# Optimization experiments

Hardware: AMD Instinct MI355X
Metric: run time of the kernel (lower is better)

## Reference

```python
import jax, jax.numpy as jnp
import numpy as np

MAX_BOXES = 50
NOOBJ_SCALE = 1.0
OBJ_SCALE = 5.0
COORD_SCALE = 1.0
CLASS_SCALE = 1.0
SIL_THRESH = 0.6


def setup_inputs() -> dict:
    key = jax.random.key(0)
    k1, k2, k3, k4 = jax.random.split(key, 4)
    nB, nA, nC, nH, nW = 32, 5, 20, 64, 64
    output = jax.random.normal(k1, (nB, nA * (5 + nC), nH, nW), jnp.float32) * 0.5
    # targets: 12 valid boxes per image, rest zero (loop-break semantics)
    K = 12
    cls = jax.random.randint(k2, (nB, MAX_BOXES, 1), 0, nC).astype(jnp.float32)
    xy = jax.random.uniform(k3, (nB, MAX_BOXES, 2), minval=0.05, maxval=0.95)
    wh = jax.random.uniform(k4, (nB, MAX_BOXES, 2), minval=0.05, maxval=0.3)
    boxes = jnp.concatenate([cls, xy, wh], axis=-1)          # [nB, 50, 5]
    valid = (jnp.arange(MAX_BOXES) < K)[None, :, None].astype(jnp.float32)
    target = (boxes * valid).reshape(nB, MAX_BOXES * 5)
    anchors = jnp.array([1.3221, 1.73145, 3.19275, 4.00944, 5.05587,
                         8.09892, 9.47112, 4.84053, 11.2364, 10.0071], jnp.float32)
    return {"output": output, "target": target, "anchors": anchors}


def _iou(b1, b2):
    # center-format boxes (cx, cy, w, h) on the last axis, broadcastable
    l = jnp.maximum(b1[..., 0] - b1[..., 2] * 0.5, b2[..., 0] - b2[..., 2] * 0.5)
    r = jnp.minimum(b1[..., 0] + b1[..., 2] * 0.5, b2[..., 0] + b2[..., 2] * 0.5)
    t = jnp.maximum(b1[..., 1] - b1[..., 3] * 0.5, b2[..., 1] - b2[..., 3] * 0.5)
    b = jnp.minimum(b1[..., 1] + b1[..., 3] * 0.5, b2[..., 1] + b2[..., 3] * 0.5)
    inter = jnp.clip(r - l, 0.0) * jnp.clip(b - t, 0.0)
    union = b1[..., 2] * b1[..., 3] + b2[..., 2] * b2[..., 3] - inter
    return inter / jnp.maximum(union, 1e-10)


def reference(output, target, anchors):
    nB, _, nH, nW = output.shape
    nA = anchors.shape[0] // 2
    nC = output.shape[1] // nA - 5
    out = output.reshape(nB, nA, 5 + nC, nH, nW)

    x = jax.nn.sigmoid(out[:, :, 0])            # [nB,nA,nH,nW]
    y = jax.nn.sigmoid(out[:, :, 1])
    w = out[:, :, 2]
    h = out[:, :, 3]
    conf = jax.nn.sigmoid(out[:, :, 4])
    cls_logits = jnp.transpose(out[:, :, 5:], (0, 1, 3, 4, 2))  # [nB,nA,nH,nW,nC]

    aw = anchors[0::2]
    ah = anchors[1::2]
    grid_x = jnp.arange(nW, dtype=output.dtype)
    grid_y = jnp.arange(nH, dtype=output.dtype)[:, None]
    px = x + grid_x
    py = y + grid_y
    pw = jnp.exp(w) * aw[None, :, None, None]
    ph = jnp.exp(h) * ah[None, :, None, None]
    # build_targets consumes pred_boxes.data -> no grad through it
    pred = jax.lax.stop_gradient(jnp.stack([px, py, pw, ph], axis=-1))  # [nB,nA,nH,nW,4]

    tgt = target.reshape(nB, -1, 5)             # (cls, x, y, w, h)
    T = tgt.shape[1]
    valid = tgt[:, :, 1] > 0
    gx = tgt[:, :, 1] * nW
    gy = tgt[:, :, 2] * nH
    gw = tgt[:, :, 3] * nW
    gh = tgt[:, :, 4] * nH
    gboxes = jnp.stack([gx, gy, gw, gh], axis=-1)  # [nB,T,4]

    # conf_mask: zero out anchors whose IoU with any gt exceeds sil_thresh
    pred_flat = pred.reshape(nB, nA * nH * nW, 4)
    ious = _iou(pred_flat[:, :, None, :], gboxes[:, None, :, :])   # [nB,nAnchors,T]
    max_iou = jnp.max(jnp.where(valid[:, None, :], ious, 0.0), axis=-1)
    conf_base = jnp.where(max_iou.reshape(nB, nA, nH, nW) > SIL_THRESH, 0.0, NOOBJ_SCALE)

    # best anchor per gt: IoU of (0,0,gw,gh) vs (0,0,aw,ah)
    inter_a = jnp.minimum(gw[..., None], aw) * jnp.minimum(gh[..., None], ah)
    iou_a = inter_a / jnp.maximum(gw[..., None] * gh[..., None] + aw * ah - inter_a, 1e-10)
    best_n = jnp.argmax(iou_a, axis=-1)          # [nB,T]

    gi = jnp.clip(jnp.floor(gx), 0, nW - 1).astype(jnp.int32)
    gj = jnp.clip(jnp.floor(gy), 0, nH - 1).astype(jnp.int32)
    bidx = jnp.arange(nB)[:, None]
    N = nB * nA * nH * nW
    flat = ((bidx * nA + best_n) * nH + gj) * nW + gi
    flat = jnp.where(valid, flat, N).reshape(-1)   # invalid gts go to dummy slot N

    def scat(base, vals):
        padded = jnp.concatenate([base.reshape(-1), jnp.zeros((1,), base.dtype)])
        return padded.at[flat].set(vals.reshape(-1))[:N].reshape(nB, nA, nH, nW)

    zeros4 = jnp.zeros((nB, nA, nH, nW), output.dtype)
    half4 = jnp.full((nB, nA, nH, nW), 0.5, output.dtype)
    # seen < 12800 branch: coord_mask all ones, tx=ty=0.5, tw=th=0 as base
    coord_mask = jnp.ones((nB, nA, nH, nW), output.dtype)
    tx = scat(half4, gx - gi.astype(output.dtype))
    ty = scat(half4, gy - gj.astype(output.dtype))
    tw = scat(zeros4, jnp.log(jnp.maximum(gw, 1e-10) / aw[best_n]))
    th = scat(zeros4, jnp.log(jnp.maximum(gh, 1e-10) / ah[best_n]))
    cls_mask = scat(zeros4, jnp.ones((nB, T), output.dtype))
    conf_mask = scat(conf_base, jnp.full((nB, T), OBJ_SCALE, output.dtype))

    pred_pad = jnp.concatenate([pred.reshape(N, 4), jnp.zeros((1, 4), pred.dtype)])
    psel = pred_pad[flat]                         # [nB*T,4]
    iou_gt = _iou(gboxes.reshape(-1, 4), psel)
    tconf = scat(zeros4, iou_gt)
    tcls = scat(zeros4, tgt[:, :, 0])

    tx, ty, tw, th, tconf = map(jax.lax.stop_gradient, (tx, ty, tw, th, tconf))

    cm = coord_mask
    loss_x = COORD_SCALE * 0.5 * jnp.sum((x * cm - tx * cm) ** 2)
    loss_y = COORD_SCALE * 0.5 * jnp.sum((y * cm - ty * cm) ** 2)
    loss_w = COORD_SCALE * 0.5 * jnp.sum((w * cm - tw * cm) ** 2)
    loss_h = COORD_SCALE * 0.5 * jnp.sum((h * cm - th * cm) ** 2)
    sq = jnp.sqrt(conf_mask)
    loss_conf = 0.5 * jnp.sum((conf * sq - tconf * sq) ** 2)
    logp = jax.nn.log_softmax(cls_logits, axis=-1)
    picked = jnp.take_along_axis(logp, tcls.astype(jnp.int32)[..., None], axis=-1)[..., 0]
    loss_cls = CLASS_SCALE * (-(picked * cls_mask).sum())
    return loss_x + loss_y + loss_w + loss_h + loss_conf + loss_cls
```

## Files before the change

### kernel.cpp

```cpp
#include <hip/hip_runtime.h>
#include <math.h>

#define NB 32
#define NA 5
#define NC 20
#define NH 64
#define NW 64
#define MAXB 50
#define CPB (NA * NH * NW)
#define NTOT (NB * CPB)
#define NBLK_DENSE (NTOT / 256)
#define NPART (NBLK_DENSE + NB)
#define SIL_THRESH 0.6f
#define OBJ_SCALE 5.0f

__device__ __forceinline__ float sigmoidf(float v) { return 1.0f / (1.0f + expf(-v)); }

__device__ __forceinline__ float iou_xywh(float x1, float y1, float w1, float h1,
                                          float x2, float y2, float w2, float h2) {
    float l = fmaxf(x1 - 0.5f * w1, x2 - 0.5f * w2);
    float r = fminf(x1 + 0.5f * w1, x2 + 0.5f * w2);
    float t = fmaxf(y1 - 0.5f * h1, y2 - 0.5f * h2);
    float b = fminf(y1 + 0.5f * h1, y2 + 0.5f * h2);
    float inter = fmaxf(r - l, 0.0f) * fmaxf(b - t, 0.0f);
    float uni = w1 * h1 + w2 * h2 - inter;
    return inter / fmaxf(uni, 1e-10f);
}

__global__ __launch_bounds__(256) void region_dense(
        const float* __restrict__ out, const float* __restrict__ target,
        const float* __restrict__ anchors, float* __restrict__ ws) {
    __shared__ float s_gx[MAXB], s_gy[MAXB], s_gw[MAXB], s_gh[MAXB];
    __shared__ int s_nv;
    __shared__ float s_aw[NA], s_ah[NA];
    __shared__ float s_part[4];

    const int tid = threadIdx.x;
    const int n = blockIdx.x * 256 + tid;
    const int b = n / CPB;

    if (tid == 0) {
        const float* tg = target + b * MAXB * 5;
        int nv = 0;
        for (int t = 0; t < MAXB; ++t) {
            float tx = tg[t * 5 + 1];
            if (tx > 0.0f) {
                s_gx[nv] = tx * NW;
                s_gy[nv] = tg[t * 5 + 2] * NH;
                s_gw[nv] = tg[t * 5 + 3] * NW;
                s_gh[nv] = tg[t * 5 + 4] * NH;
                ++nv;
            }
        }
        s_nv = nv;
    }
    if (tid < NA) { s_aw[tid] = anchors[2 * tid]; s_ah[tid] = anchors[2 * tid + 1]; }
    __syncthreads();

    const int r  = n - b * CPB;
    const int a  = r >> 12;
    const int ji = r & 4095;
    const int j  = ji >> 6;
    const int i  = ji & 63;

    const float* base = out + ((size_t)(b * 125 + a * 25) << 12) + ji;
    float xr = base[0];
    float yr = base[1 * 4096];
    float wr = base[2 * 4096];
    float hr = base[3 * 4096];
    float cr = base[4 * 4096];

    float x = sigmoidf(xr);
    float y = sigmoidf(yr);
    float conf = sigmoidf(cr);
    float px = x + (float)i;
    float py = y + (float)j;
    float pw = expf(wr) * s_aw[a];
    float ph = expf(hr) * s_ah[a];

    float maxi = 0.0f;
    const int nv = s_nv;
    for (int k = 0; k < nv; ++k) {
        float iou = iou_xywh(px, py, pw, ph, s_gx[k], s_gy[k], s_gw[k], s_gh[k]);
        maxi = fmaxf(maxi, iou);
    }
    float conf_base = (maxi > SIL_THRESH) ? 0.0f : 1.0f;

    float dx = x - 0.5f, dy = y - 0.5f;
    float v = 0.5f * (dx * dx + dy * dy + wr * wr + hr * hr)
            + 0.5f * conf_base * conf * conf;

    for (int off = 32; off; off >>= 1) v += __shfl_down(v, off);
    if ((tid & 63) == 0) s_part[tid >> 6] = v;
    __syncthreads();
    if (tid == 0)
        ws[blockIdx.x] = s_part[0] + s_part[1] + s_part[2] + s_part[3];
}

__global__ __launch_bounds__(64) void region_boxes(
        const float* __restrict__ out, const float* __restrict__ target,
        const float* __restrict__ anchors, float* __restrict__ ws) {
    const int b = blockIdx.x;
    const int tid = threadIdx.x;

    __shared__ float s_t[MAXB * 5];
    __shared__ int s_flat[MAXB];
    __shared__ float s_gx[MAXB], s_gy[MAXB], s_gw[MAXB], s_gh[MAXB];
    __shared__ int s_valid[MAXB];

    const float* tg = target + b * MAXB * 5;
    for (int idx = tid; idx < MAXB * 5; idx += 64) s_t[idx] = tg[idx];
    __syncthreads();

    float aw_[NA], ah_[NA];
    for (int q = 0; q < NA; ++q) { aw_[q] = anchors[2 * q]; ah_[q] = anchors[2 * q + 1]; }

    int myflat = -1, best_n = 0, gi = 0, gj = 0;
    float gx = 0, gy = 0, gw = 0, gh = 0, clsf = 0;
    if (tid < MAXB) {
        clsf = s_t[tid * 5 + 0];
        float xx = s_t[tid * 5 + 1];
        gx = xx * NW;
        gy = s_t[tid * 5 + 2] * NH;
        gw = s_t[tid * 5 + 3] * NW;
        gh = s_t[tid * 5 + 4] * NH;
        s_gx[tid] = gx; s_gy[tid] = gy; s_gw[tid] = gw; s_gh[tid] = gh;
        int valid = (xx > 0.0f) ? 1 : 0;
        s_valid[tid] = valid;
        if (valid) {
            float besti = -1.0f;
            for (int q = 0; q < NA; ++q) {
                float inter = fminf(gw, aw_[q]) * fminf(gh, ah_[q]);
                float iou = inter / fmaxf(gw * gh + aw_[q] * ah_[q] - inter, 1e-10f);
                if (iou > besti) { besti = iou; best_n = q; }
            }
            gi = min(max((int)floorf(gx), 0), NW - 1);
            gj = min(max((int)floorf(gy), 0), NH - 1);
            myflat = (best_n << 12) + (gj << 6) + gi;
        }
        s_flat[tid] = myflat;
    } else {
        s_flat[tid < MAXB ? tid : 0] = s_flat[tid < MAXB ? tid : 0];
    }
    __syncthreads();

    bool winner = (myflat >= 0);
    if (winner) {
        for (int t2 = tid + 1; t2 < MAXB; ++t2)
            if (s_flat[t2] == myflat) { winner = false; break; }
    }

    float delta = 0.0f;
    if (winner) {
        const float* basep = out + ((size_t)(b * 125 + best_n * 25) << 12) + (gj << 6) + gi;
        float xr = basep[0];
        float yr = basep[1 * 4096];
        float wr = basep[2 * 4096];
        float hr = basep[3 * 4096];
        float cr = basep[4 * 4096];

        float x = sigmoidf(xr);
        float y = sigmoidf(yr);
        float conf = sigmoidf(cr);
        float px = x + (float)gi;
        float py = y + (float)gj;
        float pw = expf(wr) * aw_[best_n];
        float ph = expf(hr) * ah_[best_n];

        float maxi = 0.0f;
        for (int k = 0; k < MAXB; ++k) {
            if (s_valid[k]) {
                float iou = iou_xywh(px, py, pw, ph, s_gx[k], s_gy[k], s_gw[k], s_gh[k]);
                maxi = fmaxf(maxi, iou);
            }
        }
        float conf_base = (maxi > SIL_THRESH) ? 0.0f : 1.0f;

        float txv = gx - (float)gi;
        float tyv = gy - (float)gj;
        float twv = logf(fmaxf(gw, 1e-10f) / aw_[best_n]);
        float thv = logf(fmaxf(gh, 1e-10f) / ah_[best_n]);
        float tconf = iou_xywh(gx, gy, gw, gh, px, py, pw, ph);

        float dxn = x - txv, dyn = y - tyv, dwn = wr - twv, dhn = hr - thv;
        float dxo = x - 0.5f, dyo = y - 0.5f;
        float dc = conf - tconf;

        delta = 0.5f * ((dxn * dxn - dxo * dxo) + (dyn * dyn - dyo * dyo)
                      + (dwn * dwn - wr * wr) + (dhn * dhn - hr * hr))
              + 0.5f * (OBJ_SCALE * dc * dc - conf_base * conf * conf);

        const float* cl = basep + 5 * 4096;
        int ci = (int)clsf;
        float m = -INFINITY;
        for (int c = 0; c < NC; ++c) m = fmaxf(m, cl[c * 4096]);
        float s = 0.0f;
        for (int c = 0; c < NC; ++c) s += expf(cl[c * 4096] - m);
        float picked = cl[ci * 4096] - m - logf(s);
        delta -= picked;
    }

    for (int off = 32; off; off >>= 1) delta += __shfl_down(delta, off);
    if (tid == 0) ws[NBLK_DENSE + b] = delta;
}

__global__ __launch_bounds__(256) void region_reduce(
        const float* __restrict__ ws, float* __restrict__ loss) {
    __shared__ float s_part[4];
    const int tid = threadIdx.x;
    float v = 0.0f;
    for (int idx = tid; idx < NPART; idx += 256) v += ws[idx];
    for (int off = 32; off; off >>= 1) v += __shfl_down(v, off);
    if ((tid & 63) == 0) s_part[tid >> 6] = v;
    __syncthreads();
    if (tid == 0) loss[0] = s_part[0] + s_part[1] + s_part[2] + s_part[3];
}

extern "C" void kernel_launch(void* const* d_in, const int* in_sizes, int n_in,
                              void* d_out, int out_size, void* d_ws, size_t ws_size,
                              hipStream_t stream) {
    (void)in_sizes; (void)n_in; (void)ws_size; (void)out_size;
    const float* output  = (const float*)d_in[0];
    const float* target  = (const float*)d_in[1];
    const float* anchors = (const float*)d_in[2];
    float* ws = (float*)d_ws;
    float* loss = (float*)d_out;

    region_dense<<<NBLK_DENSE, 256, 0, stream>>>(output, target, anchors, ws);
    region_boxes<<<NB, 64, 0, stream>>>(output, target, anchors, ws);
    region_reduce<<<1, 256, 0, stream>>>(ws, loss);
}
```

Before: 124.8 us.

## Precompute box edges, division-free IoU threshold test, fuse final reduction

Ground-truth boxes are now compacted once per image in a prep kernel that stores their edges and scaled areas, so dense blocks no longer rebuild them serially in thread 0. The IoU > 0.6 check becomes a division-free comparison, inter > 0.375*(area_p + area_g). Each dense thread handles two cells, and a last-block atomic counter does the final reduction, which removes the third launch. Fast intrinsics (__expf, rcp, __logf) stand in for the precise math calls, trading small accuracy differences for cheaper arithmetic.

```diff
diff --git a/kernel.cpp b/kernel.cpp
--- a/kernel.cpp
+++ b/kernel.cpp
@@ -7,16 +7,23 @@
 #define NH 64
 #define NW 64
 #define MAXB 50
-#define CPB (NA * NH * NW)
-#define NTOT (NB * CPB)
-#define NBLK_DENSE (NTOT / 256)
-#define NPART (NBLK_DENSE + NB)
-#define SIL_THRESH 0.6f
+#define CPB 20480
+#define CELLS_PER_BLOCK 512
+#define BLOCKS_PER_BATCH 40
+#define NBLK_DENSE 1280
 #define OBJ_SCALE 5.0f
-
-__device__ __forceinline__ float sigmoidf(float v) { return 1.0f / (1.0f + expf(-v)); }
-
-__device__ __forceinline__ float iou_xywh(float x1, float y1, float w1, float h1,
+#define SILC 0.375f
+
+#define WS_PART 8192
+#define NPART 1312
+#define WS_INT 9504
+#define WS_CTR (WS_INT + 32)
+
+__device__ __forceinline__ float fsig(float v) {
+    return __builtin_amdgcn_rcpf(1.0f + __expf(-v));
+}
+
+__device__ __forceinline__ float iou_full(float x1, float y1, float w1, float h1,
                                           float x2, float y2, float w2, float h2) {
     float l = fmaxf(x1 - 0.5f * w1, x2 - 0.5f * w2);
     float r = fminf(x1 + 0.5f * w1, x2 + 0.5f * w2);
@@ -27,106 +34,36 @@
     return inter / fmaxf(uni, 1e-10f);
 }
 
-__global__ __launch_bounds__(256) void region_dense(
-        const float* __restrict__ out, const float* __restrict__ target,
-        const float* __restrict__ anchors, float* __restrict__ ws) {
-    __shared__ float s_gx[MAXB], s_gy[MAXB], s_gw[MAXB], s_gh[MAXB];
-    __shared__ int s_nv;
-    __shared__ float s_aw[NA], s_ah[NA];
-    __shared__ float s_part[4];
-
-    const int tid = threadIdx.x;
-    const int n = blockIdx.x * 256 + tid;
-    const int b = n / CPB;
-
-    if (tid == 0) {
-        const float* tg = target + b * MAXB * 5;
-        int nv = 0;
-        for (int t = 0; t < MAXB; ++t) {
-            float tx = tg[t * 5 + 1];
-            if (tx > 0.0f) {
-                s_gx[nv] = tx * NW;
-                s_gy[nv] = tg[t * 5 + 2] * NH;
-                s_gw[nv] = tg[t * 5 + 3] * NW;
-                s_gh[nv] = tg[t * 5 + 4] * NH;
-                ++nv;
-            }
-        }
-        s_nv = nv;
-    }
-    if (tid < NA) { s_aw[tid] = anchors[2 * tid]; s_ah[tid] = anchors[2 * tid + 1]; }
-    __syncthreads();
-
-    const int r  = n - b * CPB;
-    const int a  = r >> 12;
-    const int ji = r & 4095;
-    const int j  = ji >> 6;
-    const int i  = ji & 63;
-
-    const float* base = out + ((size_t)(b * 125 + a * 25) << 12) + ji;
-    float xr = base[0];
-    float yr = base[1 * 4096];
-    float wr = base[2 * 4096];
-    float hr = base[3 * 4096];
-    float cr = base[4 * 4096];
-
-    float x = sigmoidf(xr);
-    float y = sigmoidf(yr);
-    float conf = sigmoidf(cr);
-    float px = x + (float)i;
-    float py = y + (float)j;
-    float pw = expf(wr) * s_aw[a];
-    float ph = expf(hr) * s_ah[a];
-
-    float maxi = 0.0f;
-    const int nv = s_nv;
-    for (int k = 0; k < nv; ++k) {
-        float iou = iou_xywh(px, py, pw, ph, s_gx[k], s_gy[k], s_gw[k], s_gh[k]);
-        maxi = fmaxf(maxi, iou);
-    }
-    float conf_base = (maxi > SIL_THRESH) ? 0.0f : 1.0f;
-
-    float dx = x - 0.5f, dy = y - 0.5f;
-    float v = 0.5f * (dx * dx + dy * dy + wr * wr + hr * hr)
-            + 0.5f * conf_base * conf * conf;
-
-    for (int off = 32; off; off >>= 1) v += __shfl_down(v, off);
-    if ((tid & 63) == 0) s_part[tid >> 6] = v;
-    __syncthreads();
-    if (tid == 0)
-        ws[blockIdx.x] = s_part[0] + s_part[1] + s_part[2] + s_part[3];
-}
-
-__global__ __launch_bounds__(64) void region_boxes(
+__global__ __launch_bounds__(64) void region_prep(
         const float* __restrict__ out, const float* __restrict__ target,
         const float* __restrict__ anchors, float* __restrict__ ws) {
     const int b = blockIdx.x;
     const int tid = threadIdx.x;
 
     __shared__ float s_t[MAXB * 5];
-    __shared__ int s_flat[MAXB];
-    __shared__ float s_gx[MAXB], s_gy[MAXB], s_gw[MAXB], s_gh[MAXB];
-    __shared__ int s_valid[MAXB];
+    __shared__ float s_e[250];
+    __shared__ int s_flat[64];
 
     const float* tg = target + b * MAXB * 5;
     for (int idx = tid; idx < MAXB * 5; idx += 64) s_t[idx] = tg[idx];
-    __syncthreads();
+    for (int idx = tid; idx < 250; idx += 64) s_e[idx] = 0.0f;
 
     float aw_[NA], ah_[NA];
     for (int q = 0; q < NA; ++q) { aw_[q] = anchors[2 * q]; ah_[q] = anchors[2 * q + 1]; }
-
-    int myflat = -1, best_n = 0, gi = 0, gj = 0;
+    __syncthreads();
+
+    bool valid = false;
+    int best_n = 0, gi = 0, gj = 0, myflat = -1;
     float gx = 0, gy = 0, gw = 0, gh = 0, clsf = 0;
+    float bl = 0, br_ = 0, bt = 0, bb_ = 0, ga = 0;
     if (tid < MAXB) {
         clsf = s_t[tid * 5 + 0];
         float xx = s_t[tid * 5 + 1];
-        gx = xx * NW;
-        gy = s_t[tid * 5 + 2] * NH;
-        gw = s_t[tid * 5 + 3] * NW;
-        gh = s_t[tid * 5 + 4] * NH;
-        s_gx[tid] = gx; s_gy[tid] = gy; s_gw[tid] = gw; s_gh[tid] = gh;
-        int valid = (xx > 0.0f) ? 1 : 0;
-        s_valid[tid] = valid;
+        gx = xx * (float)NW;
+        gy = s_t[tid * 5 + 2] * (float)NH;
+        gw = s_t[tid * 5 + 3] * (float)NW;
+        gh = s_t[tid * 5 + 4] * (float)NH;
+        valid = xx > 0.0f;
         if (valid) {
             float besti = -1.0f;
             for (int q = 0; q < NA; ++q) {
@@ -136,13 +73,29 @@
             }
             gi = min(max((int)floorf(gx), 0), NW - 1);
             gj = min(max((int)floorf(gy), 0), NH - 1);
-            myflat = (best_n << 12) + (gj << 6) + gi;
+            myflat = (best_n << 12) | (gj << 6) | gi;
+            bl = gx - 0.5f * gw; br_ = gx + 0.5f * gw;
+            bt = gy - 0.5f * gh; bb_ = gy + 0.5f * gh;
+            ga = gw * gh;
         }
-        s_flat[tid] = myflat;
-    } else {
-        s_flat[tid < MAXB ? tid : 0] = s_flat[tid < MAXB ? tid : 0];
-    }
-    __syncthreads();
+    }
+    s_flat[tid] = myflat;
+
+    unsigned long long mask = __ballot(valid);
+    int pos = __popcll(mask & ((1ull << tid) - 1ull));
+    int nv = __popcll(mask);
+    if (valid) {
+        s_e[pos] = bl; s_e[50 + pos] = br_; s_e[100 + pos] = bt;
+        s_e[150 + pos] = bb_; s_e[200 + pos] = SILC * ga;
+    }
+    __syncthreads();
+
+    float* wb = ws + b * 256;
+    for (int idx = tid; idx < 250; idx += 64) wb[idx] = s_e[idx];
+    if (tid == 0) {
+        ((int*)ws)[WS_INT + b] = nv;
+        if (b == 0) ((int*)ws)[WS_CTR] = 0;
+    }
 
     bool winner = (myflat >= 0);
     if (winner) {
@@ -159,28 +112,30 @@
         float hr = basep[3 * 4096];
         float cr = basep[4 * 4096];
 
-        float x = sigmoidf(xr);
-        float y = sigmoidf(yr);
-        float conf = sigmoidf(cr);
-        float px = x + (float)gi;
-        float py = y + (float)gj;
-        float pw = expf(wr) * aw_[best_n];
-        float ph = expf(hr) * ah_[best_n];
-
-        float maxi = 0.0f;
-        for (int k = 0; k < MAXB; ++k) {
-            if (s_valid[k]) {
-                float iou = iou_xywh(px, py, pw, ph, s_gx[k], s_gy[k], s_gw[k], s_gh[k]);
-                maxi = fmaxf(maxi, iou);
-            }
+        float x = fsig(xr), y = fsig(yr), conf = fsig(cr);
+        float aw = aw_[best_n], ah = ah_[best_n];
+        float pw = __expf(wr) * aw, ph = __expf(hr) * ah;
+        float px = x + (float)gi, py = y + (float)gj;
+        float pl = px - 0.5f * pw, pr2 = px + 0.5f * pw;
+        float pt = py - 0.5f * ph, pb2 = py + 0.5f * ph;
+        float pa375 = SILC * (pw * ph);
+
+        bool hit = false;
+        for (int k = 0; k < nv; ++k) {
+            float l = fmaxf(pl, s_e[k]);
+            float r = fminf(pr2, s_e[50 + k]);
+            float t = fmaxf(pt, s_e[100 + k]);
+            float bo = fminf(pb2, s_e[150 + k]);
+            float inter = fmaxf(r - l, 0.0f) * fmaxf(bo - t, 0.0f);
+            hit = hit || (inter > pa375 + s_e[200 + k]);
         }
-        float conf_base = (maxi > SIL_THRESH) ? 0.0f : 1.0f;
+        float cb = hit ? 0.0f : 1.0f;
 
         float txv = gx - (float)gi;
         float tyv = gy - (float)gj;
-        float twv = logf(fmaxf(gw, 1e-10f) / aw_[best_n]);
-        float thv = logf(fmaxf(gh, 1e-10f) / ah_[best_n]);
-        float tconf = iou_xywh(gx, gy, gw, gh, px, py, pw, ph);
+        float twv = __logf(fmaxf(gw, 1e-10f) / aw);
+        float thv = __logf(fmaxf(gh, 1e-10f) / ah);
+        float tconf = iou_full(gx, gy, gw, gh, px, py, pw, ph);
 
         float dxn = x - txv, dyn = y - tyv, dwn = wr - twv, dhn = hr - thv;
         float dxo = x - 0.5f, dyo = y - 0.5f;
@@ -188,32 +143,101 @@
 
         delta = 0.5f * ((dxn * dxn - dxo * dxo) + (dyn * dyn - dyo * dyo)
                       + (dwn * dwn - wr * wr) + (dhn * dhn - hr * hr))
-              + 0.5f * (OBJ_SCALE * dc * dc - conf_base * conf * conf);
+              + 0.5f * (OBJ_SCALE * dc * dc - cb * conf * conf);
 
         const float* cl = basep + 5 * 4096;
+        float lg[NC];
+        float m = -INFINITY;
+        for (int c = 0; c < NC; ++c) { lg[c] = cl[c * 4096]; m = fmaxf(m, lg[c]); }
+        float s = 0.0f;
+        for (int c = 0; c < NC; ++c) s += __expf(lg[c] - m);
         int ci = (int)clsf;
-        float m = -INFINITY;
-        for (int c = 0; c < NC; ++c) m = fmaxf(m, cl[c * 4096]);
-        float s = 0.0f;
-        for (int c = 0; c < NC; ++c) s += expf(cl[c * 4096] - m);
-        float picked = cl[ci * 4096] - m - logf(s);
-        delta -= picked;
+        delta -= (lg[ci] - m - __logf(s));
     }
 
     for (int off = 32; off; off >>= 1) delta += __shfl_down(delta, off);
-    if (tid == 0) ws[NBLK_DENSE + b] = delta;
-}
-
-__global__ __launch_bounds__(256) void region_reduce(
-        const float* __restrict__ ws, float* __restrict__ loss) {
-    __shared__ float s_part[4];
+    if (tid == 0) ws[WS_PART + NBLK_DENSE + b] = delta;
+}
+
+__global__ __launch_bounds__(256) void region_dense(
+        const float* __restrict__ out, const float* __restrict__ anchors,
+        float* __restrict__ ws, float* __restrict__ loss) {
+    __shared__ float s_box[250];
+    __shared__ int s_nv;
+    __shared__ int s_last;
+    __shared__ float s_p[4];
+
     const int tid = threadIdx.x;
+    const int blk = blockIdx.x;
+    const int b = blk / BLOCKS_PER_BATCH;
+
+    const float* wb = ws + b * 256;
+    if (tid < 250) s_box[tid] = wb[tid];
+    if (tid == 0) s_nv = ((int*)ws)[WS_INT + b];
+    __syncthreads();
+
+    const int r0 = (blk - b * BLOCKS_PER_BATCH) * CELLS_PER_BLOCK;
+    const int a = r0 >> 12;
+    const float aw = anchors[2 * a], ah = anchors[2 * a + 1];
+    const float* obase = out + ((size_t)(b * 125 + a * 25) << 12);
+    const int nv = s_nv;
+
     float v = 0.0f;
-    for (int idx = tid; idx < NPART; idx += 256) v += ws[idx];
+    #pragma unroll
+    for (int c = 0; c < 2; ++c) {
+        int cell = r0 + tid + c * 256;
+        int ji = cell & 4095;
+        int i = ji & 63, j = (ji >> 6) & 63;
+        const float* base = obase + ji;
+        float xr = base[0];
+        float yr = base[1 * 4096];
+        float wr = base[2 * 4096];
+        float hr = base[3 * 4096];
+        float cr = base[4 * 4096];
+
+        float x = fsig(xr), y = fsig(yr), conf = fsig(cr);
+        float pw = __expf(wr) * aw, ph = __expf(hr) * ah;
+        float px = x + (float)i, py = y + (float)j;
+        float pl = px - 0.5f * pw, pr2 = px + 0.5f * pw;
+        float pt = py - 0.5f * ph, pb2 = py + 0.5f * ph;
+        float pa375 = SILC * (pw * ph);
+
+        bool hit = false;
+        for (int k = 0; k < nv; ++k) {
+            float l = fmaxf(pl, s_box[k]);
+            float r = fminf(pr2, s_box[50 + k]);
+            float t = fmaxf(pt, s_box[100 + k]);
+            float bo = fminf(pb2, s_box[150 + k]);
+            float inter = fmaxf(r - l, 0.0f) * fmaxf(bo - t, 0.0f);
+            hit = hit || (inter > pa375 + s_box[200 + k]);
+        }
+        float cb = hit ? 0.0f : 1.0f;
+
+        float dx = x - 0.5f, dy = y - 0.5f;
+        v += 0.5f * (dx * dx + dy * dy + wr * wr + hr * hr)
+           + 0.5f * cb * conf * conf;
+    }
+
     for (int off = 32; off; off >>= 1) v += __shfl_down(v, off);
-    if ((tid & 63) == 0) s_part[tid >> 6] = v;
-    __syncthreads();
-    if (tid == 0) loss[0] = s_part[0] + s_part[1] + s_part[2] + s_part[3];
+    if ((tid & 63) == 0) s_p[tid >> 6] = v;
+    __syncthreads();
+    if (tid == 0) {
+        ws[WS_PART + blk] = s_p[0] + s_p[1] + s_p[2] + s_p[3];
+        __threadfence();
+        int done = atomicAdd((int*)ws + WS_CTR, 1);
+        s_last = (done == NBLK_DENSE - 1) ? 1 : 0;
+    }
+    __syncthreads();
+
+    if (s_last) {
+        __threadfence();
+        float t = 0.0f;
+        for (int idx = tid; idx < NPART; idx += 256) t += ws[WS_PART + idx];
+        for (int off = 32; off; off >>= 1) t += __shfl_down(t, off);
+        if ((tid & 63) == 0) s_p[tid >> 6] = t;
+        __syncthreads();
+        if (tid == 0) loss[0] = s_p[0] + s_p[1] + s_p[2] + s_p[3];
+    }
 }
 
 extern "C" void kernel_launch(void* const* d_in, const int* in_sizes, int n_in,
@@ -226,7 +250,6 @@
     float* ws = (float*)d_ws;
     float* loss = (float*)d_out;
 
-    region_dense<<<NBLK_DENSE, 256, 0, stream>>>(output, target, anchors, ws);
-    region_boxes<<<NB, 64, 0, stream>>>(output, target, anchors, ws);
-    region_reduce<<<1, 256, 0, stream>>>(ws, loss);
-}
+    region_prep<<<NB, 64, 0, stream>>>(output, target, anchors, ws);
+    region_dense<<<NBLK_DENSE, 256, 0, stream>>>(output, anchors, ws, loss);
+}
```

Result: slower. 128.8 us (+3.2%).
